# Performance work log

Hardware: AMD Instinct MI355X
Metric: run time of the kernel (lower is better)

Reference implementation:

```python
import jax, jax.numpy as jnp
import numpy as np

EPS = 1e-5

def _conv1d(x, w, b):
    # x: [N, Cin, L], w: [Cout, Cin, 3], SAME padding (pad=1)
    y = jax.lax.conv_general_dilated(
        x, w, window_strides=(1,), padding=((1, 1),),
        dimension_numbers=("NCH", "OIH", "NCH"))
    return y + b[None, :, None]

def _bn(x, gamma, beta, mean, var):
    # inference-mode BatchNorm1d over channel dim
    inv = gamma / jnp.sqrt(var + EPS)
    return x * inv[None, :, None] + (beta - mean * inv)[None, :, None]

def _make_params(key):
    ks = jax.random.split(key, 9)
    def w(k, o, i):
        return jax.random.normal(k, (o, i, 3), jnp.float32) * (1.0 / np.sqrt(i * 3))
    p = {}
    p["w1"], p["b1"] = w(ks[0], 128, 1), jnp.zeros((128,), jnp.float32)
    p["w2"], p["b2"] = w(ks[1], 256, 128), jnp.zeros((256,), jnp.float32)
    p["w3"], p["b3"] = w(ks[2], 256, 256), jnp.zeros((256,), jnp.float32)
    for i, c in zip((1, 2, 3), (128, 256, 256)):
        p[f"g{i}"] = jnp.ones((c,), jnp.float32)
        p[f"be{i}"] = jnp.zeros((c,), jnp.float32)
        p[f"m{i}"] = jax.random.normal(ks[2 + i], (c,), jnp.float32) * 0.1
        p[f"v{i}"] = 1.0 + 0.1 * jax.random.uniform(ks[5 + i], (c,), jnp.float32)
    return p

def setup_inputs() -> dict:
    key = jax.random.key(0)
    kx, kp = jax.random.split(key)
    inp = {"x": jax.random.normal(kx, (16, 64, 520), jnp.float32)}
    inp.update(_make_params(kp))
    return inp

def reference(x, w1, b1, w2, b2, w3, b3,
              g1, be1, m1, v1, g2, be2, m2, v2, g3, be3, m3, v3):
    B, T, D = x.shape
    h = x.reshape(B * T, 1, D)                     # fuse time into batch
    h = jax.nn.relu(_bn(_conv1d(h, w1, b1), g1, be1, m1, v1))
    h = jax.nn.relu(_bn(_conv1d(h, w2, b2), g2, be2, m2, v2))
    h = jax.nn.relu(_bn(_conv1d(h, w3, b3), g3, be3, m3, v3))
    out = h.mean(axis=-1)                          # AdaptiveAvgPool1d(1) + squeeze
    return out.reshape(B, T, -1)                   # [B, T, feature_dim]
```

## Files before the change

kernel.cpp:

```cpp
#include <hip/hip_runtime.h>
#include <hip/hip_bf16.h>

#define EPSV 1e-5f

typedef __attribute__((ext_vector_type(8))) short short8;
typedef __attribute__((ext_vector_type(4))) short short4v;
typedef __attribute__((ext_vector_type(4))) float f32x4;

static __device__ __forceinline__ short f2bf(float f) {
    unsigned int u = __builtin_bit_cast(unsigned int, f);
    unsigned int r = (u + 0x7FFFu + ((u >> 16) & 1u)) >> 16;
    return (short)(r & 0xFFFFu);
}
static __device__ __forceinline__ f32x4 zero4() { f32x4 z = {0.f, 0.f, 0.f, 0.f}; return z; }

static __device__ __forceinline__ void gload16(const void* g, void* l) {
    __builtin_amdgcn_global_load_lds((const unsigned int*)g, (unsigned int*)l, 16, 0, 0);
}

__global__ void sfe_prep(
    const float* __restrict__ w1, const float* __restrict__ b1,
    const float* __restrict__ w2, const float* __restrict__ b2,
    const float* __restrict__ w3, const float* __restrict__ b3,
    const float* __restrict__ g1, const float* __restrict__ be1,
    const float* __restrict__ m1, const float* __restrict__ v1,
    const float* __restrict__ g2, const float* __restrict__ be2,
    const float* __restrict__ m2, const float* __restrict__ v2,
    const float* __restrict__ g3, const float* __restrict__ be3,
    const float* __restrict__ m3, const float* __restrict__ v3,
    short* __restrict__ W2f, short* __restrict__ W3f,
    float* __restrict__ s1o, float* __restrict__ bb1o,
    float* __restrict__ bb2o, float* __restrict__ bb3o)
{
    int idx = blockIdx.x * 256 + threadIdx.x;
    int e = idx & 7, lane = (idx >> 3) & 63, ct = (idx >> 9) & 15;
    int lr = lane & 15, lg = lane >> 4;
    {
        int kc = idx >> 13;
        int c3 = ct * 16 + lr;
        int c2in = (kc & 7) * 32 + lg * 8 + e;
        int dk = kc >> 3;
        float s = g3[c3] / sqrtf(v3[c3] + EPSV);
        W3f[idx] = f2bf(w3[(c3 * 256 + c2in) * 3 + dk] * s);
    }
    if (idx < 98304) {
        int kc = idx >> 13;
        int c2 = ct * 16 + lr;
        int ci = (kc & 3) * 32 + lg * 8 + e;
        int dk = kc >> 2;
        float s = g2[c2] / sqrtf(v2[c2] + EPSV);
        W2f[idx] = f2bf(w2[(c2 * 128 + ci) * 3 + dk] * s);
    }
    if (idx < 128) {
        float s = g1[idx] / sqrtf(v1[idx] + EPSV);
        s1o[idx]  = s;
        bb1o[idx] = (b1[idx] - m1[idx]) * s + be1[idx];
    }
    if (idx < 256) {
        float s2 = g2[idx] / sqrtf(v2[idx] + EPSV);
        bb2o[idx] = (b2[idx] - m2[idx]) * s2 + be2[idx];
        float s3 = g3[idx] / sqrtf(v3[idx] + EPSV);
        bb3o[idx] = (b3[idx] - m3[idx]) * s3 + be3[idx];
    }
}

#define MFMA16(A, B, C) __builtin_amdgcn_mfma_f32_16x16x32_bf16(A, B, C, 0, 0, 0)

__global__ __launch_bounds__(512, 1) void sfe_l12(
    const float* __restrict__ x, const float* __restrict__ w1,
    const short* __restrict__ W2f,
    const float* __restrict__ s1a, const float* __restrict__ bb1a,
    const float* __restrict__ bb2a,
    char* __restrict__ h2g, int seq0)
{
    __shared__ __align__(16) char ring[32768];
    __shared__ __align__(16) char obuf[2][16384];
    __shared__ float xs[528];

    const int tid = threadIdx.x, lane = tid & 63, wid = tid >> 6;
    const int lr = lane & 15, lg = lane >> 4;
    const int seq = seq0 + blockIdx.x;
    char* h2b = h2g + (size_t)blockIdx.x * 270336;

    const int c4 = (tid & 31) * 4;
    float w1r[12];
    #pragma unroll
    for (int e2 = 0; e2 < 4; ++e2) {
        w1r[e2 * 3 + 0] = w1[(c4 + e2) * 3 + 0];
        w1r[e2 * 3 + 1] = w1[(c4 + e2) * 3 + 1];
        w1r[e2 * 3 + 2] = w1[(c4 + e2) * 3 + 2];
    }
    const f32x4 s1v = *reinterpret_cast<const f32x4*>(s1a + c4);
    const f32x4 b1v = *reinterpret_cast<const f32x4*>(bb1a + c4);

    short8 W2r[24];
    #pragma unroll
    for (int kc = 0; kc < 12; ++kc) {
        #pragma unroll
        for (int p = 0; p < 2; ++p)
            W2r[kc * 2 + p] = *reinterpret_cast<const short8*>(
                W2f + ((kc * 16 + wid * 2 + p) * 64 + lane) * 8);
    }
    const f32x4 bias0 = *reinterpret_cast<const f32x4*>(bb2a + (wid * 2 + 0) * 16 + lg * 4);
    const f32x4 bias1 = *reinterpret_cast<const f32x4*>(bb2a + (wid * 2 + 1) * 16 + lg * 4);

    for (int i = tid; i < 528; i += 512) {
        int l = i - 1;
        xs[i] = (l >= 0 && l < 520) ? x[(size_t)seq * 520 + l] : 0.f;
    }
    *reinterpret_cast<long long*>(ring + 28672 + tid * 8) = 0ll;
    __syncthreads();

    auto h1chunk = [&](int X) {
        int row = X * 16 + (tid >> 5);
        int rr = (row + 128) & 127;
        short4v hv;
        if (row < 520) {
            float x0 = xs[row], x1 = xs[row + 1], x2 = xs[row + 2];
            #pragma unroll
            for (int e2 = 0; e2 < 4; ++e2) {
                float a = w1r[e2 * 3] * x0 + w1r[e2 * 3 + 1] * x1 + w1r[e2 * 3 + 2] * x2;
                hv[e2] = f2bf(fmaxf(a * s1v[e2] + b1v[e2], 0.f));
            }
        } else {
            hv[0] = 0; hv[1] = 0; hv[2] = 0; hv[3] = 0;
        }
        int ch = c4 >> 3;
        *reinterpret_cast<short4v*>(
            ring + rr * 256 + ((ch ^ (row & 15)) << 4) + (c4 & 7) * 2) = hv;
    };

    h1chunk(0); h1chunk(1); h1chunk(2);
    __syncthreads();

    auto epi = [&](const f32x4& A, int p, const f32x4& bv, int jt, int b) {
        int c2b = (wid * 2 + p) * 16 + lg * 4;
        int ch = c2b >> 3;
        short4v hv;
        #pragma unroll
        for (int r = 0; r < 4; ++r) hv[r] = f2bf(fmaxf(A[r] + bv[r], 0.f));
        *reinterpret_cast<short4v*>(
            obuf[b] + (jt * 16 + lr) * 512 + ((ch ^ lr) << 4) + (c2b & 7) * 2) = hv;
    };

    for (int C = 0; C <= 32; C += 2) {
        const bool do2 = (C < 32);
        const int b = (C >> 1) & 1;
        f32x4 a00 = zero4(), a10 = zero4(), a01 = zero4(), a11 = zero4();
        const int row0base = C * 16 + lr - 1;

        if (do2) {
            #pragma unroll
            for (int kc = 0; kc < 12; ++kc) {
                int dk = kc >> 2, cc = kc & 3;
                int ch = cc * 4 + lg;
                int row0 = row0base + dk, row1 = row0 + 16;
                short8 B0 = *reinterpret_cast<const short8*>(
                    ring + ((row0 + 128) & 127) * 256 + ((ch ^ (row0 & 15)) << 4));
                short8 B1 = *reinterpret_cast<const short8*>(
                    ring + ((row1 + 128) & 127) * 256 + ((ch ^ (row1 & 15)) << 4));
                a00 = MFMA16(W2r[kc * 2 + 0], B0, a00);
                a10 = MFMA16(W2r[kc * 2 + 1], B0, a10);
                a01 = MFMA16(W2r[kc * 2 + 0], B1, a01);
                a11 = MFMA16(W2r[kc * 2 + 1], B1, a11);
            }
        } else {
            #pragma unroll
            for (int kc = 0; kc < 12; ++kc) {
                int dk = kc >> 2, cc = kc & 3;
                int ch = cc * 4 + lg;
                int row0 = row0base + dk;
                short8 B0 = *reinterpret_cast<const short8*>(
                    ring + ((row0 + 128) & 127) * 256 + ((ch ^ (row0 & 15)) << 4));
                a00 = MFMA16(W2r[kc * 2 + 0], B0, a00);
                a10 = MFMA16(W2r[kc * 2 + 1], B0, a10);
            }
        }

        if (C + 3 <= 32) h1chunk(C + 3);
        if (C + 4 <= 32) h1chunk(C + 4);

        epi(a00, 0, bias0, 0, b);
        epi(a10, 1, bias1, 0, b);
        if (do2) { epi(a01, 0, bias0, 1, b); epi(a11, 1, bias1, 1, b); }

        asm volatile("s_waitcnt lgkmcnt(0)" ::: "memory");
        __builtin_amdgcn_s_barrier();

        #pragma unroll
        for (int q = 0; q < 2; ++q) {
            int byteo = q * 8192 + tid * 16;
            int lrow = byteo >> 9;
            int grow = C * 16 + lrow;
            if (grow < 528 && (do2 || lrow < 16)) {
                short8 d = *reinterpret_cast<const short8*>(obuf[b] + byteo);
                if (grow >= 520) { short8 z = {0,0,0,0,0,0,0,0}; d = z; }
                *reinterpret_cast<short8*>(h2b + (size_t)grow * 512 + (byteo & 511)) = d;
            }
        }
    }
}

__global__ __launch_bounds__(512, 1) void sfe_l3(
    const char* __restrict__ h2g, const short* __restrict__ W3f,
    const float* __restrict__ bb3a, float* __restrict__ out, int seq0)
{
    __shared__ __align__(16) char ring[65536];

    const int tid = threadIdx.x, lane = tid & 63, wid = tid >> 6;
    const int lr = lane & 15, lg = lane >> 4;
    const int seq = seq0 + blockIdx.x;
    const char* h2b = h2g + (size_t)blockIdx.x * 270336;

    short8 W3r[48];
    #pragma unroll
    for (int kc = 0; kc < 24; ++kc) {
        #pragma unroll
        for (int p = 0; p < 2; ++p)
            W3r[kc * 2 + p] = *reinterpret_cast<const short8*>(
                W3f + ((kc * 16 + wid * 2 + p) * 64 + lane) * 8);
    }
    const f32x4 bias0 = *reinterpret_cast<const f32x4*>(bb3a + (wid * 2 + 0) * 16 + lg * 4);
    const f32x4 bias1 = *reinterpret_cast<const f32x4*>(bb3a + (wid * 2 + 1) * 16 + lg * 4);
    f32x4 pool0 = zero4(), pool1 = zero4();

    auto stage = [&](int X) {
        int Xc = X > 32 ? 32 : X;
        gload16(h2b + Xc * 8192 + tid * 16, ring + (X & 7) * 8192 + tid * 16);
    };

    *reinterpret_cast<f32x4*>(ring + 57344 + tid * 16) = zero4();
    stage(0); stage(1); stage(2); stage(3); stage(4);
    asm volatile("s_waitcnt vmcnt(2) lgkmcnt(0)" ::: "memory");
    __builtin_amdgcn_s_barrier();

    for (int C = 0; C <= 32; C += 2) {
        stage(C + 5); stage(C + 6);
        __builtin_amdgcn_sched_barrier(0);

        const bool do2 = (C < 32);
        f32x4 a00 = zero4(), a10 = zero4(), a01 = zero4(), a11 = zero4();
        const int row0base = C * 16 + lr - 1;

        if (do2) {
            #pragma unroll
            for (int kc = 0; kc < 24; ++kc) {
                int dk = kc >> 3, cc = kc & 7;
                int ch = cc * 4 + lg;
                int row0 = row0base + dk, row1 = row0 + 16;
                short8 B0 = *reinterpret_cast<const short8*>(
                    ring + ((row0 + 128) & 127) * 512 + ((ch ^ (row0 & 15)) << 4));
                short8 B1 = *reinterpret_cast<const short8*>(
                    ring + ((row1 + 128) & 127) * 512 + ((ch ^ (row1 & 15)) << 4));
                a00 = MFMA16(W3r[kc * 2 + 0], B0, a00);
                a10 = MFMA16(W3r[kc * 2 + 1], B0, a10);
                a01 = MFMA16(W3r[kc * 2 + 0], B1, a01);
                a11 = MFMA16(W3r[kc * 2 + 1], B1, a11);
            }
        } else {
            #pragma unroll
            for (int kc = 0; kc < 24; ++kc) {
                int dk = kc >> 3, cc = kc & 7;
                int ch = cc * 4 + lg;
                int row0 = row0base + dk;
                short8 B0 = *reinterpret_cast<const short8*>(
                    ring + ((row0 + 128) & 127) * 512 + ((ch ^ (row0 & 15)) << 4));
                a00 = MFMA16(W3r[kc * 2 + 0], B0, a00);
                a10 = MFMA16(W3r[kc * 2 + 1], B0, a10);
            }
        }

        {
            bool v0 = (C * 16 + lr) < 520;
            f32x4 t0, t1;
            #pragma unroll
            for (int r = 0; r < 4; ++r) {
                t0[r] = fmaxf(a00[r] + bias0[r], 0.f);
                t1[r] = fmaxf(a10[r] + bias1[r], 0.f);
            }
            pool0 += v0 ? t0 : zero4();
            pool1 += v0 ? t1 : zero4();
            if (do2) {
                #pragma unroll
                for (int r = 0; r < 4; ++r) {
                    t0[r] = fmaxf(a01[r] + bias0[r], 0.f);
                    t1[r] = fmaxf(a11[r] + bias1[r], 0.f);
                }
                pool0 += t0;
                pool1 += t1;
            }
        }

        asm volatile("s_waitcnt vmcnt(2) lgkmcnt(0)" ::: "memory");
        __builtin_amdgcn_s_barrier();
    }

    asm volatile("s_waitcnt vmcnt(0)" ::: "memory");

    #pragma unroll
    for (int d = 1; d < 16; d <<= 1) {
        #pragma unroll
        for (int r = 0; r < 4; ++r) {
            pool0[r] += __shfl_xor(pool0[r], d, 64);
            pool1[r] += __shfl_xor(pool1[r], d, 64);
        }
    }
    if (lr == 0) {
        f32x4 o0, o1;
        #pragma unroll
        for (int r = 0; r < 4; ++r) { o0[r] = pool0[r] * (1.f / 520.f); o1[r] = pool1[r] * (1.f / 520.f); }
        *reinterpret_cast<f32x4*>(out + (size_t)seq * 256 + (wid * 2 + 0) * 16 + lg * 4) = o0;
        *reinterpret_cast<f32x4*>(out + (size_t)seq * 256 + (wid * 2 + 1) * 16 + lg * 4) = o1;
    }
}

extern "C" void kernel_launch(void* const* d_in, const int* in_sizes, int n_in,
                              void* d_out, int out_size, void* d_ws, size_t ws_size,
                              hipStream_t stream) {
    (void)n_in; (void)out_size;
    const float* x   = (const float*)d_in[0];
    const float* w1  = (const float*)d_in[1];
    const float* b1  = (const float*)d_in[2];
    const float* w2  = (const float*)d_in[3];
    const float* b2  = (const float*)d_in[4];
    const float* w3  = (const float*)d_in[5];
    const float* b3  = (const float*)d_in[6];
    const float* g1  = (const float*)d_in[7];
    const float* be1 = (const float*)d_in[8];
    const float* m1  = (const float*)d_in[9];
    const float* v1  = (const float*)d_in[10];
    const float* g2  = (const float*)d_in[11];
    const float* be2 = (const float*)d_in[12];
    const float* m2  = (const float*)d_in[13];
    const float* v2  = (const float*)d_in[14];
    const float* g3  = (const float*)d_in[15];
    const float* be3 = (const float*)d_in[16];
    const float* m3  = (const float*)d_in[17];
    const float* v3  = (const float*)d_in[18];

    char* ws = (char*)d_ws;
    short* W2f  = (short*)(ws);
    short* W3f  = (short*)(ws + 196608);
    float* s1o  = (float*)(ws + 589824);
    float* bb1o = (float*)(ws + 590336);
    float* bb2o = (float*)(ws + 590848);
    float* bb3o = (float*)(ws + 591872);
    char*  h2g  = ws + (1 << 20);

    int nseq = in_sizes[0] / 520;
    size_t h2cap = ws_size > (size_t)(1 << 20) ? ws_size - (1 << 20) : 0;
    int maxseq = (int)(h2cap / 270336);
    if (maxseq < 1) maxseq = 1;
    if (maxseq > nseq) maxseq = nseq;

    sfe_prep<<<768, 256, 0, stream>>>(w1, b1, w2, b2, w3, b3,
                                      g1, be1, m1, v1, g2, be2, m2, v2,
                                      g3, be3, m3, v3,
                                      W2f, W3f, s1o, bb1o, bb2o, bb3o);
    for (int s0 = 0; s0 < nseq; s0 += maxseq) {
        int n = (nseq - s0) < maxseq ? (nseq - s0) : maxseq;
        sfe_l12<<<n, 512, 0, stream>>>(x, w1, W2f, s1o, bb1o, bb2o, h2g, s0);
        sfe_l3 <<<n, 512, 0, stream>>>(h2g, W3f, bb3o, (float*)d_out, s0);
    }
}
```

Measured before the change: 526.7 us.

## Stream conv weights from global per k-chunk instead of holding them in registers

The layer-2 and layer-3 kernels no longer preload their full weight slices into register arrays (24 and 48 short8 values per lane). Each k-chunk iteration now reloads its two weight fragments from global memory, and launch bounds move from 1 to 4 blocks per CU. This frees a large number of VGPRs so more waves can be resident at once. In exchange every MFMA step now waits on global loads that are repeated for every row chunk, and LDS use per block may still cap how many blocks actually fit.

```diff
diff --git a/kernel.cpp b/kernel.cpp
--- a/kernel.cpp
+++ b/kernel.cpp
@@ -16,6 +16,9 @@
 
 static __device__ __forceinline__ void gload16(const void* g, void* l) {
     __builtin_amdgcn_global_load_lds((const unsigned int*)g, (unsigned int*)l, 16, 0, 0);
+}
+static __device__ __forceinline__ short8 ldg8(const short* p) {
+    return *reinterpret_cast<const short8*>(p);
 }
 
 __global__ void sfe_prep(
@@ -66,7 +69,7 @@
 
 #define MFMA16(A, B, C) __builtin_amdgcn_mfma_f32_16x16x32_bf16(A, B, C, 0, 0, 0)
 
-__global__ __launch_bounds__(512, 1) void sfe_l12(
+__global__ __launch_bounds__(512, 4) void sfe_l12(
     const float* __restrict__ x, const float* __restrict__ w1,
     const short* __restrict__ W2f,
     const float* __restrict__ s1a, const float* __restrict__ bb1a,
@@ -93,14 +96,7 @@
     const f32x4 s1v = *reinterpret_cast<const f32x4*>(s1a + c4);
     const f32x4 b1v = *reinterpret_cast<const f32x4*>(bb1a + c4);
 
-    short8 W2r[24];
-    #pragma unroll
-    for (int kc = 0; kc < 12; ++kc) {
-        #pragma unroll
-        for (int p = 0; p < 2; ++p)
-            W2r[kc * 2 + p] = *reinterpret_cast<const short8*>(
-                W2f + ((kc * 16 + wid * 2 + p) * 64 + lane) * 8);
-    }
+    const short* W2base = W2f + (wid * 2) * 512 + lane * 8;
     const f32x4 bias0 = *reinterpret_cast<const f32x4*>(bb2a + (wid * 2 + 0) * 16 + lg * 4);
     const f32x4 bias1 = *reinterpret_cast<const f32x4*>(bb2a + (wid * 2 + 1) * 16 + lg * 4);
 
@@ -155,14 +151,16 @@
                 int dk = kc >> 2, cc = kc & 3;
                 int ch = cc * 4 + lg;
                 int row0 = row0base + dk, row1 = row0 + 16;
+                short8 A0 = ldg8(W2base + kc * 8192);
+                short8 A1 = ldg8(W2base + kc * 8192 + 512);
                 short8 B0 = *reinterpret_cast<const short8*>(
                     ring + ((row0 + 128) & 127) * 256 + ((ch ^ (row0 & 15)) << 4));
                 short8 B1 = *reinterpret_cast<const short8*>(
                     ring + ((row1 + 128) & 127) * 256 + ((ch ^ (row1 & 15)) << 4));
-                a00 = MFMA16(W2r[kc * 2 + 0], B0, a00);
-                a10 = MFMA16(W2r[kc * 2 + 1], B0, a10);
-                a01 = MFMA16(W2r[kc * 2 + 0], B1, a01);
-                a11 = MFMA16(W2r[kc * 2 + 1], B1, a11);
+                a00 = MFMA16(A0, B0, a00);
+                a10 = MFMA16(A1, B0, a10);
+                a01 = MFMA16(A0, B1, a01);
+                a11 = MFMA16(A1, B1, a11);
             }
         } else {
             #pragma unroll
@@ -170,10 +168,12 @@
                 int dk = kc >> 2, cc = kc & 3;
                 int ch = cc * 4 + lg;
                 int row0 = row0base + dk;
+                short8 A0 = ldg8(W2base + kc * 8192);
+                short8 A1 = ldg8(W2base + kc * 8192 + 512);
                 short8 B0 = *reinterpret_cast<const short8*>(
                     ring + ((row0 + 128) & 127) * 256 + ((ch ^ (row0 & 15)) << 4));
-                a00 = MFMA16(W2r[kc * 2 + 0], B0, a00);
-                a10 = MFMA16(W2r[kc * 2 + 1], B0, a10);
+                a00 = MFMA16(A0, B0, a00);
+                a10 = MFMA16(A1, B0, a10);
             }
         }
 
@@ -201,7 +201,7 @@
     }
 }
 
-__global__ __launch_bounds__(512, 1) void sfe_l3(
+__global__ __launch_bounds__(512, 4) void sfe_l3(
     const char* __restrict__ h2g, const short* __restrict__ W3f,
     const float* __restrict__ bb3a, float* __restrict__ out, int seq0)
 {
@@ -212,14 +212,7 @@
     const int seq = seq0 + blockIdx.x;
     const char* h2b = h2g + (size_t)blockIdx.x * 270336;
 
-    short8 W3r[48];
-    #pragma unroll
-    for (int kc = 0; kc < 24; ++kc) {
-        #pragma unroll
-        for (int p = 0; p < 2; ++p)
-            W3r[kc * 2 + p] = *reinterpret_cast<const short8*>(
-                W3f + ((kc * 16 + wid * 2 + p) * 64 + lane) * 8);
-    }
+    const short* W3base = W3f + (wid * 2) * 512 + lane * 8;
     const f32x4 bias0 = *reinterpret_cast<const f32x4*>(bb3a + (wid * 2 + 0) * 16 + lg * 4);
     const f32x4 bias1 = *reinterpret_cast<const f32x4*>(bb3a + (wid * 2 + 1) * 16 + lg * 4);
     f32x4 pool0 = zero4(), pool1 = zero4();
@@ -248,14 +241,16 @@
                 int dk = kc >> 3, cc = kc & 7;
                 int ch = cc * 4 + lg;
                 int row0 = row0base + dk, row1 = row0 + 16;
+                short8 A0 = ldg8(W3base + kc * 8192);
+                short8 A1 = ldg8(W3base + kc * 8192 + 512);
                 short8 B0 = *reinterpret_cast<const short8*>(
                     ring + ((row0 + 128) & 127) * 512 + ((ch ^ (row0 & 15)) << 4));
                 short8 B1 = *reinterpret_cast<const short8*>(
                     ring + ((row1 + 128) & 127) * 512 + ((ch ^ (row1 & 15)) << 4));
-                a00 = MFMA16(W3r[kc * 2 + 0], B0, a00);
-                a10 = MFMA16(W3r[kc * 2 + 1], B0, a10);
-                a01 = MFMA16(W3r[kc * 2 + 0], B1, a01);
-                a11 = MFMA16(W3r[kc * 2 + 1], B1, a11);
+                a00 = MFMA16(A0, B0, a00);
+                a10 = MFMA16(A1, B0, a10);
+                a01 = MFMA16(A0, B1, a01);
+                a11 = MFMA16(A1, B1, a11);
             }
         } else {
             #pragma unroll
@@ -263,10 +258,12 @@
                 int dk = kc >> 3, cc = kc & 7;
                 int ch = cc * 4 + lg;
                 int row0 = row0base + dk;
+                short8 A0 = ldg8(W3base + kc * 8192);
+                short8 A1 = ldg8(W3base + kc * 8192 + 512);
                 short8 B0 = *reinterpret_cast<const short8*>(
                     ring + ((row0 + 128) & 127) * 512 + ((ch ^ (row0 & 15)) << 4));
-                a00 = MFMA16(W3r[kc * 2 + 0], B0, a00);
-                a10 = MFMA16(W3r[kc * 2 + 1], B0, a10);
+                a00 = MFMA16(A0, B0, a00);
+                a10 = MFMA16(A1, B0, a10);
             }
         }
 
```

Result: slower. 1.058 ms (+100.9%).

## Split each sequence's output channels across two 256-thread blocks

Applied to the files above, without the earlier changes.

Each sequence is now handled by two blocks of 256 threads, each computing half of the output channels for layers 2 and 3. This doubles the grid and raises occupancy per CU (launch bounds 256 threads with 3 or 2 blocks per CU), so more waves are available to hide latency. The cost is duplicated work: each half-block recomputes layer 1 and re-stages the full h2 input into LDS, which doubles the reads of the shared activations.

```diff
diff --git a/kernel.cpp b/kernel.cpp
--- a/kernel.cpp
+++ b/kernel.cpp
@@ -66,7 +66,7 @@
 
 #define MFMA16(A, B, C) __builtin_amdgcn_mfma_f32_16x16x32_bf16(A, B, C, 0, 0, 0)
 
-__global__ __launch_bounds__(512, 1) void sfe_l12(
+__global__ __launch_bounds__(256, 3) void sfe_l12(
     const float* __restrict__ x, const float* __restrict__ w1,
     const short* __restrict__ W2f,
     const float* __restrict__ s1a, const float* __restrict__ bb1a,
@@ -74,15 +74,18 @@
     char* __restrict__ h2g, int seq0)
 {
     __shared__ __align__(16) char ring[32768];
-    __shared__ __align__(16) char obuf[2][16384];
+    __shared__ __align__(16) char obuf[2][8192];
     __shared__ float xs[528];
 
     const int tid = threadIdx.x, lane = tid & 63, wid = tid >> 6;
     const int lr = lane & 15, lg = lane >> 4;
-    const int seq = seq0 + blockIdx.x;
-    char* h2b = h2g + (size_t)blockIdx.x * 270336;
+    const int bi = blockIdx.x;
+    const int seq = seq0 + (bi >> 1);
+    const int ch2 = bi & 1;
+    char* h2b = h2g + (size_t)(bi >> 1) * 270336;
 
     const int c4 = (tid & 31) * 4;
+    const int chw = c4 >> 3;
     float w1r[12];
     #pragma unroll
     for (int e2 = 0; e2 < 4; ++e2) {
@@ -99,48 +102,51 @@
         #pragma unroll
         for (int p = 0; p < 2; ++p)
             W2r[kc * 2 + p] = *reinterpret_cast<const short8*>(
-                W2f + ((kc * 16 + wid * 2 + p) * 64 + lane) * 8);
-    }
-    const f32x4 bias0 = *reinterpret_cast<const f32x4*>(bb2a + (wid * 2 + 0) * 16 + lg * 4);
-    const f32x4 bias1 = *reinterpret_cast<const f32x4*>(bb2a + (wid * 2 + 1) * 16 + lg * 4);
-
-    for (int i = tid; i < 528; i += 512) {
+                W2f + ((kc * 16 + ch2 * 8 + wid * 2 + p) * 64 + lane) * 8);
+    }
+    const f32x4 bias0 = *reinterpret_cast<const f32x4*>(bb2a + (ch2 * 8 + wid * 2 + 0) * 16 + lg * 4);
+    const f32x4 bias1 = *reinterpret_cast<const f32x4*>(bb2a + (ch2 * 8 + wid * 2 + 1) * 16 + lg * 4);
+
+    for (int i = tid; i < 528; i += 256) {
         int l = i - 1;
         xs[i] = (l >= 0 && l < 520) ? x[(size_t)seq * 520 + l] : 0.f;
     }
-    *reinterpret_cast<long long*>(ring + 28672 + tid * 8) = 0ll;
+    *reinterpret_cast<f32x4*>(ring + 28672 + tid * 16) = zero4();
     __syncthreads();
 
     auto h1chunk = [&](int X) {
-        int row = X * 16 + (tid >> 5);
-        int rr = (row + 128) & 127;
-        short4v hv;
-        if (row < 520) {
-            float x0 = xs[row], x1 = xs[row + 1], x2 = xs[row + 2];
-            #pragma unroll
-            for (int e2 = 0; e2 < 4; ++e2) {
-                float a = w1r[e2 * 3] * x0 + w1r[e2 * 3 + 1] * x1 + w1r[e2 * 3 + 2] * x2;
-                hv[e2] = f2bf(fmaxf(a * s1v[e2] + b1v[e2], 0.f));
-            }
-        } else {
-            hv[0] = 0; hv[1] = 0; hv[2] = 0; hv[3] = 0;
-        }
-        int ch = c4 >> 3;
-        *reinterpret_cast<short4v*>(
-            ring + rr * 256 + ((ch ^ (row & 15)) << 4) + (c4 & 7) * 2) = hv;
+        #pragma unroll
+        for (int rh = 0; rh < 2; ++rh) {
+            int row = X * 16 + rh * 8 + (tid >> 5);
+            int rr = row & 127;
+            short4v hv;
+            if (row < 520) {
+                float x0 = xs[row], x1 = xs[row + 1], x2 = xs[row + 2];
+                #pragma unroll
+                for (int e2 = 0; e2 < 4; ++e2) {
+                    float a = w1r[e2 * 3] * x0 + w1r[e2 * 3 + 1] * x1 + w1r[e2 * 3 + 2] * x2;
+                    hv[e2] = f2bf(fmaxf(a * s1v[e2] + b1v[e2], 0.f));
+                }
+            } else {
+                hv[0] = 0; hv[1] = 0; hv[2] = 0; hv[3] = 0;
+            }
+            *reinterpret_cast<short4v*>(
+                ring + rr * 256 + ((chw ^ (row & 15)) << 4) + (c4 & 7) * 2) = hv;
+        }
     };
 
     h1chunk(0); h1chunk(1); h1chunk(2);
     __syncthreads();
 
     auto epi = [&](const f32x4& A, int p, const f32x4& bv, int jt, int b) {
-        int c2b = (wid * 2 + p) * 16 + lg * 4;
-        int ch = c2b >> 3;
+        int c2b = (ch2 * 8 + wid * 2 + p) * 16 + lg * 4;
+        int chl = c2b & 127;
+        int chv = chl >> 3;
         short4v hv;
         #pragma unroll
         for (int r = 0; r < 4; ++r) hv[r] = f2bf(fmaxf(A[r] + bv[r], 0.f));
         *reinterpret_cast<short4v*>(
-            obuf[b] + (jt * 16 + lr) * 512 + ((ch ^ lr) << 4) + (c2b & 7) * 2) = hv;
+            obuf[b] + (jt * 16 + lr) * 256 + ((chv ^ lr) << 4) + (chl & 7) * 2) = hv;
     };
 
     for (int C = 0; C <= 32; C += 2) {
@@ -189,19 +195,20 @@
 
         #pragma unroll
         for (int q = 0; q < 2; ++q) {
-            int byteo = q * 8192 + tid * 16;
-            int lrow = byteo >> 9;
+            int byteo = q * 4096 + tid * 16;
+            int lrow = byteo >> 8;
             int grow = C * 16 + lrow;
             if (grow < 528 && (do2 || lrow < 16)) {
                 short8 d = *reinterpret_cast<const short8*>(obuf[b] + byteo);
                 if (grow >= 520) { short8 z = {0,0,0,0,0,0,0,0}; d = z; }
-                *reinterpret_cast<short8*>(h2b + (size_t)grow * 512 + (byteo & 511)) = d;
-            }
-        }
-    }
-}
-
-__global__ __launch_bounds__(512, 1) void sfe_l3(
+                *reinterpret_cast<short8*>(
+                    h2b + (size_t)grow * 512 + ch2 * 256 + (byteo & 255)) = d;
+            }
+        }
+    }
+}
+
+__global__ __launch_bounds__(256, 2) void sfe_l3(
     const char* __restrict__ h2g, const short* __restrict__ W3f,
     const float* __restrict__ bb3a, float* __restrict__ out, int seq0)
 {
@@ -209,8 +216,10 @@
 
     const int tid = threadIdx.x, lane = tid & 63, wid = tid >> 6;
     const int lr = lane & 15, lg = lane >> 4;
-    const int seq = seq0 + blockIdx.x;
-    const char* h2b = h2g + (size_t)blockIdx.x * 270336;
+    const int bi = blockIdx.x;
+    const int seq = seq0 + (bi >> 1);
+    const int ch2 = bi & 1;
+    const char* h2b = h2g + (size_t)(bi >> 1) * 270336;
 
     short8 W3r[48];
     #pragma unroll
@@ -218,20 +227,25 @@
         #pragma unroll
         for (int p = 0; p < 2; ++p)
             W3r[kc * 2 + p] = *reinterpret_cast<const short8*>(
-                W3f + ((kc * 16 + wid * 2 + p) * 64 + lane) * 8);
-    }
-    const f32x4 bias0 = *reinterpret_cast<const f32x4*>(bb3a + (wid * 2 + 0) * 16 + lg * 4);
-    const f32x4 bias1 = *reinterpret_cast<const f32x4*>(bb3a + (wid * 2 + 1) * 16 + lg * 4);
+                W3f + ((kc * 16 + ch2 * 8 + wid * 2 + p) * 64 + lane) * 8);
+    }
+    const f32x4 bias0 = *reinterpret_cast<const f32x4*>(bb3a + (ch2 * 8 + wid * 2 + 0) * 16 + lg * 4);
+    const f32x4 bias1 = *reinterpret_cast<const f32x4*>(bb3a + (ch2 * 8 + wid * 2 + 1) * 16 + lg * 4);
     f32x4 pool0 = zero4(), pool1 = zero4();
 
     auto stage = [&](int X) {
         int Xc = X > 32 ? 32 : X;
-        gload16(h2b + Xc * 8192 + tid * 16, ring + (X & 7) * 8192 + tid * 16);
+        #pragma unroll
+        for (int q = 0; q < 2; ++q)
+            gload16(h2b + Xc * 8192 + q * 4096 + tid * 16,
+                    ring + (X & 7) * 8192 + q * 4096 + tid * 16);
     };
 
-    *reinterpret_cast<f32x4*>(ring + 57344 + tid * 16) = zero4();
+    #pragma unroll
+    for (int q = 0; q < 2; ++q)
+        *reinterpret_cast<f32x4*>(ring + 57344 + q * 4096 + tid * 16) = zero4();
     stage(0); stage(1); stage(2); stage(3); stage(4);
-    asm volatile("s_waitcnt vmcnt(2) lgkmcnt(0)" ::: "memory");
+    asm volatile("s_waitcnt vmcnt(4) lgkmcnt(0)" ::: "memory");
     __builtin_amdgcn_s_barrier();
 
     for (int C = 0; C <= 32; C += 2) {
@@ -291,7 +305,7 @@
             }
         }
 
-        asm volatile("s_waitcnt vmcnt(2) lgkmcnt(0)" ::: "memory");
+        asm volatile("s_waitcnt vmcnt(4) lgkmcnt(0)" ::: "memory");
         __builtin_amdgcn_s_barrier();
     }
 
@@ -309,8 +323,8 @@
         f32x4 o0, o1;
         #pragma unroll
         for (int r = 0; r < 4; ++r) { o0[r] = pool0[r] * (1.f / 520.f); o1[r] = pool1[r] * (1.f / 520.f); }
-        *reinterpret_cast<f32x4*>(out + (size_t)seq * 256 + (wid * 2 + 0) * 16 + lg * 4) = o0;
-        *reinterpret_cast<f32x4*>(out + (size_t)seq * 256 + (wid * 2 + 1) * 16 + lg * 4) = o1;
+        *reinterpret_cast<f32x4*>(out + (size_t)seq * 256 + (ch2 * 8 + wid * 2 + 0) * 16 + lg * 4) = o0;
+        *reinterpret_cast<f32x4*>(out + (size_t)seq * 256 + (ch2 * 8 + wid * 2 + 1) * 16 + lg * 4) = o1;
     }
 }
 
@@ -359,7 +373,7 @@
                                       W2f, W3f, s1o, bb1o, bb2o, bb3o);
     for (int s0 = 0; s0 < nseq; s0 += maxseq) {
         int n = (nseq - s0) < maxseq ? (nseq - s0) : maxseq;
-        sfe_l12<<<n, 512, 0, stream>>>(x, w1, W2f, s1o, bb1o, bb2o, h2g, s0);
-        sfe_l3 <<<n, 512, 0, stream>>>(h2g, W3f, bb3o, (float*)d_out, s0);
-    }
-}
+        sfe_l12<<<n * 2, 256, 0, stream>>>(x, w1, W2f, s1o, bb1o, bb2o, h2g, s0);
+        sfe_l3 <<<n * 2, 256, 0, stream>>>(h2g, W3f, bb3o, (float*)d_out, s0);
+    }
+}
```

New measurement: 550.6 us. +4.5%, slower.

## Split layer-2 conv across four blocks per sequence by output-channel quarter

Applied to the files above, without the earlier changes.

sfe_l12 now launches four 256-thread blocks per sequence instead of one 512-thread block. Each block owns 64 of the 256 layer-2 output channels, holds fewer weight registers and uses a smaller output staging buffer, with launch bounds set for three blocks per CU. The goal is more resident waves to hide latency and better overlap across the GPU. The cost is that every block recomputes the full layer-1 activations, four times the redundant layer-1 work. The layer-3 ring read swizzle also changes from row&15 to row&7, which only stays correct if the unseen staging writes use the same pattern.

```diff
diff --git a/kernel.cpp b/kernel.cpp
--- a/kernel.cpp
+++ b/kernel.cpp
@@ -66,7 +66,7 @@
 
 #define MFMA16(A, B, C) __builtin_amdgcn_mfma_f32_16x16x32_bf16(A, B, C, 0, 0, 0)
 
-__global__ __launch_bounds__(512, 1) void sfe_l12(
+__global__ __launch_bounds__(256, 3) void sfe_l12(
     const float* __restrict__ x, const float* __restrict__ w1,
     const short* __restrict__ W2f,
     const float* __restrict__ s1a, const float* __restrict__ bb1a,
@@ -74,15 +74,18 @@
     char* __restrict__ h2g, int seq0)
 {
     __shared__ __align__(16) char ring[32768];
-    __shared__ __align__(16) char obuf[2][16384];
+    __shared__ __align__(16) char obuf[2][4096];
     __shared__ float xs[528];
 
     const int tid = threadIdx.x, lane = tid & 63, wid = tid >> 6;
     const int lr = lane & 15, lg = lane >> 4;
-    const int seq = seq0 + blockIdx.x;
-    char* h2b = h2g + (size_t)blockIdx.x * 270336;
+    const int bi = blockIdx.x;
+    const int seq = seq0 + (bi >> 2);
+    const int qtr = bi & 3;
+    char* h2b = h2g + (size_t)(bi >> 2) * 270336;
 
     const int c4 = (tid & 31) * 4;
+    const int chw = c4 >> 3;
     float w1r[12];
     #pragma unroll
     for (int e2 = 0; e2 < 4; ++e2) {
@@ -93,60 +96,59 @@
     const f32x4 s1v = *reinterpret_cast<const f32x4*>(s1a + c4);
     const f32x4 b1v = *reinterpret_cast<const f32x4*>(bb1a + c4);
 
-    short8 W2r[24];
+    const int ct = qtr * 4 + wid;
+    short8 W2r[12];
     #pragma unroll
-    for (int kc = 0; kc < 12; ++kc) {
-        #pragma unroll
-        for (int p = 0; p < 2; ++p)
-            W2r[kc * 2 + p] = *reinterpret_cast<const short8*>(
-                W2f + ((kc * 16 + wid * 2 + p) * 64 + lane) * 8);
-    }
-    const f32x4 bias0 = *reinterpret_cast<const f32x4*>(bb2a + (wid * 2 + 0) * 16 + lg * 4);
-    const f32x4 bias1 = *reinterpret_cast<const f32x4*>(bb2a + (wid * 2 + 1) * 16 + lg * 4);
-
-    for (int i = tid; i < 528; i += 512) {
+    for (int kc = 0; kc < 12; ++kc)
+        W2r[kc] = *reinterpret_cast<const short8*>(
+            W2f + ((kc * 16 + ct) * 64 + lane) * 8);
+    const f32x4 bias0 = *reinterpret_cast<const f32x4*>(bb2a + ct * 16 + lg * 4);
+
+    for (int i = tid; i < 528; i += 256) {
         int l = i - 1;
         xs[i] = (l >= 0 && l < 520) ? x[(size_t)seq * 520 + l] : 0.f;
     }
-    *reinterpret_cast<long long*>(ring + 28672 + tid * 8) = 0ll;
+    *reinterpret_cast<f32x4*>(ring + 28672 + tid * 16) = zero4();
     __syncthreads();
 
     auto h1chunk = [&](int X) {
-        int row = X * 16 + (tid >> 5);
-        int rr = (row + 128) & 127;
-        short4v hv;
-        if (row < 520) {
-            float x0 = xs[row], x1 = xs[row + 1], x2 = xs[row + 2];
-            #pragma unroll
-            for (int e2 = 0; e2 < 4; ++e2) {
-                float a = w1r[e2 * 3] * x0 + w1r[e2 * 3 + 1] * x1 + w1r[e2 * 3 + 2] * x2;
-                hv[e2] = f2bf(fmaxf(a * s1v[e2] + b1v[e2], 0.f));
-            }
-        } else {
-            hv[0] = 0; hv[1] = 0; hv[2] = 0; hv[3] = 0;
-        }
-        int ch = c4 >> 3;
-        *reinterpret_cast<short4v*>(
-            ring + rr * 256 + ((ch ^ (row & 15)) << 4) + (c4 & 7) * 2) = hv;
+        #pragma unroll
+        for (int rh = 0; rh < 2; ++rh) {
+            int row = X * 16 + rh * 8 + (tid >> 5);
+            int rr = row & 127;
+            short4v hv;
+            if (row < 520) {
+                float x0 = xs[row], x1 = xs[row + 1], x2 = xs[row + 2];
+                #pragma unroll
+                for (int e2 = 0; e2 < 4; ++e2) {
+                    float a = w1r[e2 * 3] * x0 + w1r[e2 * 3 + 1] * x1 + w1r[e2 * 3 + 2] * x2;
+                    hv[e2] = f2bf(fmaxf(a * s1v[e2] + b1v[e2], 0.f));
+                }
+            } else {
+                hv[0] = 0; hv[1] = 0; hv[2] = 0; hv[3] = 0;
+            }
+            *reinterpret_cast<short4v*>(
+                ring + rr * 256 + ((chw ^ (row & 15)) << 4) + (c4 & 7) * 2) = hv;
+        }
     };
 
     h1chunk(0); h1chunk(1); h1chunk(2);
     __syncthreads();
 
-    auto epi = [&](const f32x4& A, int p, const f32x4& bv, int jt, int b) {
-        int c2b = (wid * 2 + p) * 16 + lg * 4;
-        int ch = c2b >> 3;
+    auto epi = [&](const f32x4& A, int jt, int b) {
+        int c2b = ct * 16 + lg * 4;
+        int chl = (c2b >> 3) & 7;
         short4v hv;
         #pragma unroll
-        for (int r = 0; r < 4; ++r) hv[r] = f2bf(fmaxf(A[r] + bv[r], 0.f));
+        for (int r = 0; r < 4; ++r) hv[r] = f2bf(fmaxf(A[r] + bias0[r], 0.f));
         *reinterpret_cast<short4v*>(
-            obuf[b] + (jt * 16 + lr) * 512 + ((ch ^ lr) << 4) + (c2b & 7) * 2) = hv;
+            obuf[b] + (jt * 16 + lr) * 128 + ((chl ^ (lr & 7)) << 4) + (c2b & 7) * 2) = hv;
     };
 
     for (int C = 0; C <= 32; C += 2) {
         const bool do2 = (C < 32);
         const int b = (C >> 1) & 1;
-        f32x4 a00 = zero4(), a10 = zero4(), a01 = zero4(), a11 = zero4();
+        f32x4 a0 = zero4(), a1 = zero4();
         const int row0base = C * 16 + lr - 1;
 
         if (do2) {
@@ -159,10 +161,8 @@
                     ring + ((row0 + 128) & 127) * 256 + ((ch ^ (row0 & 15)) << 4));
                 short8 B1 = *reinterpret_cast<const short8*>(
                     ring + ((row1 + 128) & 127) * 256 + ((ch ^ (row1 & 15)) << 4));
-                a00 = MFMA16(W2r[kc * 2 + 0], B0, a00);
-                a10 = MFMA16(W2r[kc * 2 + 1], B0, a10);
-                a01 = MFMA16(W2r[kc * 2 + 0], B1, a01);
-                a11 = MFMA16(W2r[kc * 2 + 1], B1, a11);
+                a0 = MFMA16(W2r[kc], B0, a0);
+                a1 = MFMA16(W2r[kc], B1, a1);
             }
         } else {
             #pragma unroll
@@ -172,30 +172,28 @@
                 int row0 = row0base + dk;
                 short8 B0 = *reinterpret_cast<const short8*>(
                     ring + ((row0 + 128) & 127) * 256 + ((ch ^ (row0 & 15)) << 4));
-                a00 = MFMA16(W2r[kc * 2 + 0], B0, a00);
-                a10 = MFMA16(W2r[kc * 2 + 1], B0, a10);
+                a0 = MFMA16(W2r[kc], B0, a0);
             }
         }
 
         if (C + 3 <= 32) h1chunk(C + 3);
         if (C + 4 <= 32) h1chunk(C + 4);
 
-        epi(a00, 0, bias0, 0, b);
-        epi(a10, 1, bias1, 0, b);
-        if (do2) { epi(a01, 0, bias0, 1, b); epi(a11, 1, bias1, 1, b); }
+        epi(a0, 0, b);
+        if (do2) epi(a1, 1, b);
 
         asm volatile("s_waitcnt lgkmcnt(0)" ::: "memory");
         __builtin_amdgcn_s_barrier();
 
-        #pragma unroll
-        for (int q = 0; q < 2; ++q) {
-            int byteo = q * 8192 + tid * 16;
-            int lrow = byteo >> 9;
+        {
+            int byteo = tid * 16;
+            int lrow = tid >> 3;
             int grow = C * 16 + lrow;
             if (grow < 528 && (do2 || lrow < 16)) {
                 short8 d = *reinterpret_cast<const short8*>(obuf[b] + byteo);
                 if (grow >= 520) { short8 z = {0,0,0,0,0,0,0,0}; d = z; }
-                *reinterpret_cast<short8*>(h2b + (size_t)grow * 512 + (byteo & 511)) = d;
+                *reinterpret_cast<short8*>(
+                    h2b + (size_t)grow * 512 + qtr * 128 + (tid & 7) * 16) = d;
             }
         }
     }
@@ -249,9 +247,9 @@
                 int ch = cc * 4 + lg;
                 int row0 = row0base + dk, row1 = row0 + 16;
                 short8 B0 = *reinterpret_cast<const short8*>(
-                    ring + ((row0 + 128) & 127) * 512 + ((ch ^ (row0 & 15)) << 4));
+                    ring + ((row0 + 128) & 127) * 512 + ((ch ^ (row0 & 7)) << 4));
                 short8 B1 = *reinterpret_cast<const short8*>(
-                    ring + ((row1 + 128) & 127) * 512 + ((ch ^ (row1 & 15)) << 4));
+                    ring + ((row1 + 128) & 127) * 512 + ((ch ^ (row1 & 7)) << 4));
                 a00 = MFMA16(W3r[kc * 2 + 0], B0, a00);
                 a10 = MFMA16(W3r[kc * 2 + 1], B0, a10);
                 a01 = MFMA16(W3r[kc * 2 + 0], B1, a01);
@@ -264,7 +262,7 @@
                 int ch = cc * 4 + lg;
                 int row0 = row0base + dk;
                 short8 B0 = *reinterpret_cast<const short8*>(
-                    ring + ((row0 + 128) & 127) * 512 + ((ch ^ (row0 & 15)) << 4));
+                    ring + ((row0 + 128) & 127) * 512 + ((ch ^ (row0 & 7)) << 4));
                 a00 = MFMA16(W3r[kc * 2 + 0], B0, a00);
                 a10 = MFMA16(W3r[kc * 2 + 1], B0, a10);
             }
@@ -359,7 +357,7 @@
                                       W2f, W3f, s1o, bb1o, bb2o, bb3o);
     for (int s0 = 0; s0 < nseq; s0 += maxseq) {
         int n = (nseq - s0) < maxseq ? (nseq - s0) : maxseq;
-        sfe_l12<<<n, 512, 0, stream>>>(x, w1, W2f, s1o, bb1o, bb2o, h2g, s0);
+        sfe_l12<<<n * 4, 256, 0, stream>>>(x, w1, W2f, s1o, bb1o, bb2o, h2g, s0);
         sfe_l3 <<<n, 512, 0, stream>>>(h2g, W3f, bb3o, (float*)d_out, s0);
     }
 }
```

Result: slower. 548.4 us (+4.1%).
